# Performance work log

Hardware: AMD Instinct MI355X
Metric: run time of the kernel (lower is better)

The kernel has to match this reference:

```python
import jax, jax.numpy as jnp
import numpy as np

N = 50000      # nodes
E = 800000     # edges (avg degree 16)
D_IN, D_H, D_OUT = 128, 256, 128


def setup_inputs() -> dict:
    key = jax.random.key(0)
    ks = jax.random.split(key, 8)
    x = jax.random.normal(ks[0], (N, D_IN), dtype=jnp.float32)
    edge_index = jax.random.randint(ks[1], (2, E), 0, N, dtype=jnp.int64)
    s1 = 1.0 / np.sqrt(D_IN).astype(np.float32)
    s2 = 1.0 / np.sqrt(D_H).astype(np.float32)
    return {
        "x": x,
        "edge_index": edge_index,
        "W1l": jax.random.normal(ks[2], (D_H, D_IN), jnp.float32) * s1,
        "b1l": jnp.zeros((D_H,), jnp.float32),
        "W1r": jax.random.normal(ks[3], (D_H, D_IN), jnp.float32) * s1,
        "W2l": jax.random.normal(ks[4], (D_OUT, D_H), jnp.float32) * s2,
        "b2l": jnp.zeros((D_OUT,), jnp.float32),
        "W2r": jax.random.normal(ks[5], (D_OUT, D_H), jnp.float32) * s2,
    }


def sage_conv(x, src, dst, Wl, bl, Wr):
    # mean-aggregate source features into destination nodes
    agg = jax.ops.segment_sum(x[src], dst, num_segments=N)           # [N, d_in]
    deg = jax.ops.segment_sum(jnp.ones((src.shape[0],), x.dtype), dst, num_segments=N)
    mean = agg / jnp.maximum(deg, 1.0)[:, None]
    # lin_l(mean_agg) + lin_r(x_root); lin_r has no bias (PyG SAGEConv default)
    return mean @ Wl.T + bl + x @ Wr.T


def reference(x, edge_index, W1l, b1l, W1r, W2l, b2l, W2r):
    src, dst = edge_index[0], edge_index[1]
    h = sage_conv(x, src, dst, W1l, b1l, W1r)
    h = jax.nn.relu(h)  # dropout inactive in eval mode
    return sage_conv(h, src, dst, W2l, b2l, W2r)
```

## Files before the change

kernel.cpp:

```cpp
#include <hip/hip_runtime.h>


typedef __attribute__((ext_vector_type(8))) short bf16x8;
typedef __attribute__((ext_vector_type(4))) float floatx4;

__device__ inline unsigned short f2b(float f) {
  unsigned int x = __float_as_uint(f);
  unsigned int r = (x + 0x7fffu + ((x >> 16) & 1u)) >> 16;
  return (unsigned short)r;
}
__device__ inline float blo(unsigned int u) { return __uint_as_float(u << 16); }
__device__ inline float bhi(unsigned int u) { return __uint_as_float(u & 0xffff0000u); }

#define ACC8(A, u)                                            \
  {                                                           \
    A[0] += blo((u).x); A[1] += bhi((u).x);                   \
    A[2] += blo((u).y); A[3] += bhi((u).y);                   \
    A[4] += blo((u).z); A[5] += bhi((u).z);                   \
    A[6] += blo((u).w); A[7] += bhi((u).w);                   \
  }

__global__ void prep_kernel(const float* __restrict__ x,
                            const float* __restrict__ W1l, const float* __restrict__ W1r,
                            const float* __restrict__ W2l, const float* __restrict__ W2r,
                            unsigned short* __restrict__ Wc1, unsigned short* __restrict__ Wc2,
                            unsigned short* __restrict__ A1,
                            int* __restrict__ cnt, int* __restrict__ off, int N, int E) {
  int i = blockIdx.x * blockDim.x + threadIdx.x;
  if (i < 65536) {
    int j = i >> 8, k = i & 255;
    float v1 = (k < 128) ? W1l[j * 128 + k] : W1r[j * 128 + (k - 128)];
    Wc1[i] = f2b(v1);
    float v2 = (j < 128) ? W2l[j * 256 + k] : W2r[(j - 128) * 256 + k];
    Wc2[i] = f2b(v2);
  }
  if (i < N) cnt[i] = 0;
  if (i == 0) off[N] = E;
  if (i < N * 32) {
    int n = i >> 5, c = (i & 31) * 4;
    float4 v = *(const float4*)(x + (size_t)n * 128 + c);
    uint2 p;
    p.x = (unsigned int)f2b(v.x) | ((unsigned int)f2b(v.y) << 16);
    p.y = (unsigned int)f2b(v.z) | ((unsigned int)f2b(v.w) << 16);
    *(uint2*)(A1 + (size_t)n * 256 + 128 + c) = p;
  }
}

__global__ void hist_kernel(const int* __restrict__ dst, int* __restrict__ cnt,
                            int* __restrict__ rank, int E) {
  int i = blockIdx.x * blockDim.x + threadIdx.x;
  int e = i * 4;
  if (e + 3 < E) {
    int4 d = *(const int4*)(dst + e);
    int4 r;
    r.x = atomicAdd(&cnt[d.x], 1);
    r.y = atomicAdd(&cnt[d.y], 1);
    r.z = atomicAdd(&cnt[d.z], 1);
    r.w = atomicAdd(&cnt[d.w], 1);
    *(int4*)(rank + e) = r;
  } else {
    for (; e < E; e++) rank[e] = atomicAdd(&cnt[dst[e]], 1);
  }
}

__global__ __launch_bounds__(1024) void scan_blocks_kernel(const int* __restrict__ cnt,
                                                           int* __restrict__ off,
                                                           int* __restrict__ bsum, int N) {
  __shared__ int wsum[16];
  __shared__ int wincl[16];
  const int tid = threadIdx.x;
  const int lane = tid & 63;
  const int wv = tid >> 6;
  const int i = blockIdx.x * 1024 + tid;
  const int v = (i < N) ? cnt[i] : 0;
  int s = v;
#pragma unroll
  for (int o = 1; o < 64; o <<= 1) {
    int t = __shfl_up(s, o, 64);
    if (lane >= o) s += t;
  }
  if (lane == 63) wsum[wv] = s;
  __syncthreads();
  if (tid < 16) {
    int ws = wsum[tid];
#pragma unroll
    for (int o = 1; o < 16; o <<= 1) {
      int t = __shfl_up(ws, o, 16);
      if ((tid & 15) >= o) ws += t;
    }
    wincl[tid] = ws;
  }
  __syncthreads();
  const int wo = wv ? wincl[wv - 1] : 0;
  if (i < N) off[i] = wo + s - v;
  if (tid == 1023) bsum[blockIdx.x] = wo + s;
}

__global__ __launch_bounds__(1024) void scan_add_kernel(int* __restrict__ off,
                                                        const int* __restrict__ bsum, int N, int SB) {
  __shared__ int bofs[64];
  const int tid = threadIdx.x;
  if (tid < 64) {
    int v = (tid < SB) ? bsum[tid] : 0;
    int s = v;
#pragma unroll
    for (int o = 1; o < 64; o <<= 1) {
      int t = __shfl_up(s, o, 64);
      if (tid >= o) s += t;
    }
    bofs[tid] = s - v;
  }
  __syncthreads();
  int i = blockIdx.x * 1024 + tid;
  if (i < N) off[i] = off[i] + bofs[blockIdx.x];
}

__global__ void fill_kernel(const int* __restrict__ src, const int* __restrict__ dst,
                            const int* __restrict__ rank, const int* __restrict__ off,
                            int* __restrict__ csr, int E) {
  int i = blockIdx.x * blockDim.x + threadIdx.x;
  int e = i * 4;
  if (e + 3 < E) {
    int4 d = *(const int4*)(dst + e);
    int4 r = *(const int4*)(rank + e);
    int4 s = *(const int4*)(src + e);
    csr[off[d.x] + r.x] = s.x;
    csr[off[d.y] + r.y] = s.y;
    csr[off[d.z] + r.z] = s.z;
    csr[off[d.w] + r.w] = s.w;
  } else {
    for (; e < E; e++) csr[off[dst[e]] + rank[e]] = src[e];
  }
}

__global__ void gather1_kernel(const unsigned short* __restrict__ feat,
                               const int* __restrict__ csr, const int* __restrict__ off,
                               unsigned short* __restrict__ ob, int N) {
  int wid = (blockIdx.x * blockDim.x + threadIdx.x) >> 6;
  if (wid >= N) return;
  const int lane = threadIdx.x & 63;
  const int slot = lane >> 3;
  const int j = lane & 7;
  const int c0 = j * 8;
  const int s0 = off[wid], s1 = off[wid + 1];
  float a[16] = {};
  int e = s0 + slot;
  for (; e + 8 < s1; e += 16) {
    int i0 = csr[e], i1 = csr[e + 8];
    uint4 u0 = *(const uint4*)(feat + (size_t)i0 * 256 + c0);
    uint4 v0 = *(const uint4*)(feat + (size_t)i0 * 256 + 64 + c0);
    uint4 u1 = *(const uint4*)(feat + (size_t)i1 * 256 + c0);
    uint4 v1 = *(const uint4*)(feat + (size_t)i1 * 256 + 64 + c0);
    ACC8(a, u0); ACC8((a + 8), v0);
    ACC8(a, u1); ACC8((a + 8), v1);
  }
  for (; e < s1; e += 8) {
    int i0 = csr[e];
    uint4 u0 = *(const uint4*)(feat + (size_t)i0 * 256 + c0);
    uint4 v0 = *(const uint4*)(feat + (size_t)i0 * 256 + 64 + c0);
    ACC8(a, u0); ACC8((a + 8), v0);
  }
#pragma unroll
  for (int k = 0; k < 16; k++) {
    a[k] += __shfl_xor(a[k], 8, 64);
    a[k] += __shfl_xor(a[k], 16, 64);
    a[k] += __shfl_xor(a[k], 32, 64);
  }
  if (slot == 0) {
    const float inv = 1.0f / fmaxf((float)(s1 - s0), 1.0f);
    uint4 p;
    p.x = (unsigned int)f2b(a[0] * inv) | ((unsigned int)f2b(a[1] * inv) << 16);
    p.y = (unsigned int)f2b(a[2] * inv) | ((unsigned int)f2b(a[3] * inv) << 16);
    p.z = (unsigned int)f2b(a[4] * inv) | ((unsigned int)f2b(a[5] * inv) << 16);
    p.w = (unsigned int)f2b(a[6] * inv) | ((unsigned int)f2b(a[7] * inv) << 16);
    *(uint4*)(ob + (size_t)wid * 256 + c0) = p;
    p.x = (unsigned int)f2b(a[8] * inv) | ((unsigned int)f2b(a[9] * inv) << 16);
    p.y = (unsigned int)f2b(a[10] * inv) | ((unsigned int)f2b(a[11] * inv) << 16);
    p.z = (unsigned int)f2b(a[12] * inv) | ((unsigned int)f2b(a[13] * inv) << 16);
    p.w = (unsigned int)f2b(a[14] * inv) | ((unsigned int)f2b(a[15] * inv) << 16);
    *(uint4*)(ob + (size_t)wid * 256 + 64 + c0) = p;
  }
}

__global__ void gather2_kernel(const unsigned short* __restrict__ t,
                               const int* __restrict__ csr, const int* __restrict__ off,
                               float* __restrict__ out, int N) {
  int wid = (blockIdx.x * blockDim.x + threadIdx.x) >> 6;
  if (wid >= N) return;
  const int lane = threadIdx.x & 63;
  const int slot = lane >> 3;
  const int j = lane & 7;
  const int c0 = j * 8;
  const int s0 = off[wid], s1 = off[wid + 1];
  float a[16] = {};
  int e = s0 + slot;
  for (; e + 8 < s1; e += 16) {
    int i0 = csr[e], i1 = csr[e + 8];
    uint4 u0 = *(const uint4*)(t + (size_t)i0 * 128 + c0);
    uint4 v0 = *(const uint4*)(t + (size_t)i0 * 128 + 64 + c0);
    uint4 u1 = *(const uint4*)(t + (size_t)i1 * 128 + c0);
    uint4 v1 = *(const uint4*)(t + (size_t)i1 * 128 + 64 + c0);
    ACC8(a, u0); ACC8((a + 8), v0);
    ACC8(a, u1); ACC8((a + 8), v1);
  }
  for (; e < s1; e += 8) {
    int i0 = csr[e];
    uint4 u0 = *(const uint4*)(t + (size_t)i0 * 128 + c0);
    uint4 v0 = *(const uint4*)(t + (size_t)i0 * 128 + 64 + c0);
    ACC8(a, u0); ACC8((a + 8), v0);
  }
#pragma unroll
  for (int k = 0; k < 16; k++) {
    a[k] += __shfl_xor(a[k], 8, 64);
    a[k] += __shfl_xor(a[k], 16, 64);
    a[k] += __shfl_xor(a[k], 32, 64);
  }
  if (slot == 0) {
    const float inv = 1.0f / fmaxf((float)(s1 - s0), 1.0f);
    float4* o0 = (float4*)(out + (size_t)wid * 128 + c0);
    float4* o1 = (float4*)(out + (size_t)wid * 128 + 64 + c0);
    float4 r0 = o0[0], r1 = o0[1], r2 = o1[0], r3 = o1[1];
    r0.x += a[0] * inv;  r0.y += a[1] * inv;  r0.z += a[2] * inv;  r0.w += a[3] * inv;
    r1.x += a[4] * inv;  r1.y += a[5] * inv;  r1.z += a[6] * inv;  r1.w += a[7] * inv;
    r2.x += a[8] * inv;  r2.y += a[9] * inv;  r2.z += a[10] * inv; r2.w += a[11] * inv;
    r3.x += a[12] * inv; r3.y += a[13] * inv; r3.z += a[14] * inv; r3.w += a[15] * inv;
    o0[0] = r0; o0[1] = r1; o1[0] = r2; o1[1] = r3;
  }
}

__global__ __launch_bounds__(512, 4)
void gemm1(const unsigned short* __restrict__ A, const unsigned short* __restrict__ Wc1,
           const float* __restrict__ b1, unsigned short* __restrict__ H, int M) {
  constexpr int LDA = 264;
  __shared__ __align__(16) unsigned short As[64 * LDA];
  const int t = threadIdx.x;
  const int lane = t & 63;
  const int wave = t >> 6;
  const int wn = wave * 32;
  const int l15 = lane & 15;
  const int quad = lane >> 4;
  const int m_blk = blockIdx.x * 64;

  bf16x8 wr[2][8];
#pragma unroll
  for (int nt = 0; nt < 2; nt++) {
    const unsigned short* wp = Wc1 + (size_t)(wn + nt * 16 + l15) * 256 + quad * 8;
#pragma unroll
    for (int c = 0; c < 8; c++) wr[nt][c] = *(const bf16x8*)(wp + c * 32);
  }
  const float bv0 = b1[wn + l15];
  const float bv1 = b1[wn + 16 + l15];

#pragma unroll
  for (int i = 0; i < 4; i++) {
    int idx = t + 512 * i;
    int row = idx >> 5, cc = (idx & 31) * 8;
    int ar = m_blk + row;
    if (ar >= M) ar = M - 1;
    *(uint4*)(As + row * LDA + cc) = *(const uint4*)(A + (size_t)ar * 256 + cc);
  }
  __syncthreads();

  floatx4 acc[4][2] = {};
#pragma unroll
  for (int c = 0; c < 8; c++) {
    bf16x8 af[4];
#pragma unroll
    for (int mt = 0; mt < 4; mt++)
      af[mt] = *(const bf16x8*)(As + (mt * 16 + l15) * LDA + c * 32 + quad * 8);
#pragma unroll
    for (int mt = 0; mt < 4; mt++) {
      acc[mt][0] = __builtin_amdgcn_mfma_f32_16x16x32_bf16(af[mt], wr[0][c], acc[mt][0], 0, 0, 0);
      acc[mt][1] = __builtin_amdgcn_mfma_f32_16x16x32_bf16(af[mt], wr[1][c], acc[mt][1], 0, 0, 0);
    }
  }

#pragma unroll
  for (int mt = 0; mt < 4; mt++) {
#pragma unroll
    for (int nt = 0; nt < 2; nt++) {
      const int j = wn + nt * 16 + l15;
      const float bv = nt ? bv1 : bv0;
#pragma unroll
      for (int r = 0; r < 4; r++) {
        const int node = m_blk + mt * 16 + quad * 4 + r;
        if (node < M) H[(size_t)node * 256 + j] = f2b(fmaxf(acc[mt][nt][r] + bv, 0.f));
      }
    }
  }
}

__global__ __launch_bounds__(512, 4)
void gemm2(const unsigned short* __restrict__ H, const unsigned short* __restrict__ Wc2,
           const float* __restrict__ b2, unsigned short* __restrict__ tb,
           float* __restrict__ out, int M) {
  constexpr int LDA = 264;
  __shared__ __align__(16) unsigned short As[64 * LDA];
  const int t = threadIdx.x;
  const int lane = t & 63;
  const int wave = t >> 6;
  const int wn = wave * 32;
  const int l15 = lane & 15;
  const int quad = lane >> 4;
  const int m_blk = blockIdx.x * 64;

  bf16x8 wr[2][8];
#pragma unroll
  for (int nt = 0; nt < 2; nt++) {
    const unsigned short* wp = Wc2 + (size_t)(wn + nt * 16 + l15) * 256 + quad * 8;
#pragma unroll
    for (int c = 0; c < 8; c++) wr[nt][c] = *(const bf16x8*)(wp + c * 32);
  }
  const float bv0 = (wn >= 128) ? b2[wn - 128 + l15] : 0.f;
  const float bv1 = (wn >= 128) ? b2[wn - 112 + l15] : 0.f;

#pragma unroll
  for (int i = 0; i < 4; i++) {
    int idx = t + 512 * i;
    int row = idx >> 5, cc = (idx & 31) * 8;
    int ar = m_blk + row;
    if (ar >= M) ar = M - 1;
    *(uint4*)(As + row * LDA + cc) = *(const uint4*)(H + (size_t)ar * 256 + cc);
  }
  __syncthreads();

  floatx4 acc[4][2] = {};
#pragma unroll
  for (int c = 0; c < 8; c++) {
    bf16x8 af[4];
#pragma unroll
    for (int mt = 0; mt < 4; mt++)
      af[mt] = *(const bf16x8*)(As + (mt * 16 + l15) * LDA + c * 32 + quad * 8);
#pragma unroll
    for (int mt = 0; mt < 4; mt++) {
      acc[mt][0] = __builtin_amdgcn_mfma_f32_16x16x32_bf16(af[mt], wr[0][c], acc[mt][0], 0, 0, 0);
      acc[mt][1] = __builtin_amdgcn_mfma_f32_16x16x32_bf16(af[mt], wr[1][c], acc[mt][1], 0, 0, 0);
    }
  }

#pragma unroll
  for (int mt = 0; mt < 4; mt++) {
#pragma unroll
    for (int nt = 0; nt < 2; nt++) {
      const int j = wn + nt * 16 + l15;
      const float bv = nt ? bv1 : bv0;
#pragma unroll
      for (int r = 0; r < 4; r++) {
        const int node = m_blk + mt * 16 + quad * 4 + r;
        if (node >= M) continue;
        const float v = acc[mt][nt][r];
        if (j < 128) {
          tb[(size_t)node * 128 + j] = f2b(v);
        } else {
          out[(size_t)node * 128 + (j - 128)] = v + bv;
        }
      }
    }
  }
}

extern "C" void kernel_launch(void* const* d_in, const int* in_sizes, int n_in,
                              void* d_out, int out_size, void* d_ws, size_t ws_size,
                              hipStream_t stream) {
  const float* x   = (const float*)d_in[0];
  const int*  eidx = (const int*)d_in[1];
  const float* W1l = (const float*)d_in[2];
  const float* b1l = (const float*)d_in[3];
  const float* W1r = (const float*)d_in[4];
  const float* W2l = (const float*)d_in[5];
  const float* b2l = (const float*)d_in[6];
  const float* W2r = (const float*)d_in[7];
  float* out = (float*)d_out;

  const int N = in_sizes[0] / 128;
  const int E = in_sizes[1] / 2;
  const int* src = eidx;
  const int* dst = eidx + E;

  int* cnt  = (int*)d_ws;
  int* off  = cnt + N;
  int* bsum = off + N + 1;
  int* rank = bsum + 64;
  int* csr  = rank + E;
  size_t ioff = ((size_t)(N + N + 1 + 64 + 2 * E) * 4 + 15) & ~(size_t)15;
  unsigned short* A1  = (unsigned short*)((char*)d_ws + ioff);
  unsigned short* h   = A1 + (size_t)N * 256;
  unsigned short* tb  = h + (size_t)N * 256;
  unsigned short* Wc1 = tb + (size_t)N * 128;
  unsigned short* Wc2 = Wc1 + 65536;

  const int SB = (N + 1023) / 1024;

  prep_kernel<<<(N * 32 + 255) / 256, 256, 0, stream>>>(x, W1l, W1r, W2l, W2r,
                                                        Wc1, Wc2, A1, cnt, off, N, E);
  hist_kernel<<<(E / 4 + 255) / 256, 256, 0, stream>>>(dst, cnt, rank, E);
  scan_blocks_kernel<<<SB, 1024, 0, stream>>>(cnt, off, bsum, N);
  scan_add_kernel<<<SB, 1024, 0, stream>>>(off, bsum, N, SB);
  fill_kernel<<<(E / 4 + 255) / 256, 256, 0, stream>>>(src, dst, rank, off, csr, E);

  const int gblocks = (N + 3) / 4;
  gather1_kernel<<<gblocks, 256, 0, stream>>>(A1 + 128, csr, off, A1, N);

  const int mblocks = (N + 63) / 64;
  gemm1<<<mblocks, 512, 0, stream>>>(A1, Wc1, b1l, h, N);
  gemm2<<<mblocks, 512, 0, stream>>>(h, Wc2, b2l, tb, out, N);

  gather2_kernel<<<gblocks, 256, 0, stream>>>(tb, csr, off, out, N);
}
```

Baseline: 275.8 us.

## Fuse both GEMMs via shared-memory hidden tile and restructure gathers per-lane

The two GEMM kernels become one: the ReLU'd hidden tile is written to a second shared-memory buffer and fed straight into the second GEMM, so the bf16 hidden matrix no longer makes a round trip through global memory. The gather kernels also change layout. Each wave now loads a chunk of up to 64 neighbor indices at once, broadcasts them with shuffles, and has every lane read a 4-byte column pair per neighbor. This removes the cross-slot shuffle reductions but processes only one neighbor row per load step, unrolled by 4. The fused kernel doubles shared memory per block, which may lower occupancy.

```diff
diff --git a/kernel.cpp b/kernel.cpp
--- a/kernel.cpp
+++ b/kernel.cpp
@@ -11,14 +11,6 @@
 }
 __device__ inline float blo(unsigned int u) { return __uint_as_float(u << 16); }
 __device__ inline float bhi(unsigned int u) { return __uint_as_float(u & 0xffff0000u); }
-
-#define ACC8(A, u)                                            \
-  {                                                           \
-    A[0] += blo((u).x); A[1] += bhi((u).x);                   \
-    A[2] += blo((u).y); A[3] += bhi((u).y);                   \
-    A[4] += blo((u).z); A[5] += bhi((u).z);                   \
-    A[6] += blo((u).w); A[7] += bhi((u).w);                   \
-  }
 
 __global__ void prep_kernel(const float* __restrict__ x,
                             const float* __restrict__ W1l, const float* __restrict__ W1r,
@@ -139,47 +131,35 @@
   int wid = (blockIdx.x * blockDim.x + threadIdx.x) >> 6;
   if (wid >= N) return;
   const int lane = threadIdx.x & 63;
-  const int slot = lane >> 3;
-  const int j = lane & 7;
-  const int c0 = j * 8;
   const int s0 = off[wid], s1 = off[wid + 1];
-  float a[16] = {};
-  int e = s0 + slot;
-  for (; e + 8 < s1; e += 16) {
-    int i0 = csr[e], i1 = csr[e + 8];
-    uint4 u0 = *(const uint4*)(feat + (size_t)i0 * 256 + c0);
-    uint4 v0 = *(const uint4*)(feat + (size_t)i0 * 256 + 64 + c0);
-    uint4 u1 = *(const uint4*)(feat + (size_t)i1 * 256 + c0);
-    uint4 v1 = *(const uint4*)(feat + (size_t)i1 * 256 + 64 + c0);
-    ACC8(a, u0); ACC8((a + 8), v0);
-    ACC8(a, u1); ACC8((a + 8), v1);
-  }
-  for (; e < s1; e += 8) {
-    int i0 = csr[e];
-    uint4 u0 = *(const uint4*)(feat + (size_t)i0 * 256 + c0);
-    uint4 v0 = *(const uint4*)(feat + (size_t)i0 * 256 + 64 + c0);
-    ACC8(a, u0); ACC8((a + 8), v0);
-  }
-#pragma unroll
-  for (int k = 0; k < 16; k++) {
-    a[k] += __shfl_xor(a[k], 8, 64);
-    a[k] += __shfl_xor(a[k], 16, 64);
-    a[k] += __shfl_xor(a[k], 32, 64);
-  }
-  if (slot == 0) {
-    const float inv = 1.0f / fmaxf((float)(s1 - s0), 1.0f);
-    uint4 p;
-    p.x = (unsigned int)f2b(a[0] * inv) | ((unsigned int)f2b(a[1] * inv) << 16);
-    p.y = (unsigned int)f2b(a[2] * inv) | ((unsigned int)f2b(a[3] * inv) << 16);
-    p.z = (unsigned int)f2b(a[4] * inv) | ((unsigned int)f2b(a[5] * inv) << 16);
-    p.w = (unsigned int)f2b(a[6] * inv) | ((unsigned int)f2b(a[7] * inv) << 16);
-    *(uint4*)(ob + (size_t)wid * 256 + c0) = p;
-    p.x = (unsigned int)f2b(a[8] * inv) | ((unsigned int)f2b(a[9] * inv) << 16);
-    p.y = (unsigned int)f2b(a[10] * inv) | ((unsigned int)f2b(a[11] * inv) << 16);
-    p.z = (unsigned int)f2b(a[12] * inv) | ((unsigned int)f2b(a[13] * inv) << 16);
-    p.w = (unsigned int)f2b(a[14] * inv) | ((unsigned int)f2b(a[15] * inv) << 16);
-    *(uint4*)(ob + (size_t)wid * 256 + 64 + c0) = p;
-  }
+  float a0 = 0.f, a1 = 0.f;
+  for (int base = s0; base < s1; base += 64) {
+    const int cnt = min(64, s1 - base);
+    int my = (lane < cnt) ? csr[base + lane] : 0;
+    int k = 0;
+    for (; k + 4 <= cnt; k += 4) {
+      int i0 = __shfl(my, k);
+      int i1 = __shfl(my, k + 1);
+      int i2 = __shfl(my, k + 2);
+      int i3 = __shfl(my, k + 3);
+      unsigned u0 = ((const unsigned*)(feat + (size_t)i0 * 256))[lane];
+      unsigned u1 = ((const unsigned*)(feat + (size_t)i1 * 256))[lane];
+      unsigned u2 = ((const unsigned*)(feat + (size_t)i2 * 256))[lane];
+      unsigned u3 = ((const unsigned*)(feat + (size_t)i3 * 256))[lane];
+      a0 += blo(u0); a1 += bhi(u0);
+      a0 += blo(u1); a1 += bhi(u1);
+      a0 += blo(u2); a1 += bhi(u2);
+      a0 += blo(u3); a1 += bhi(u3);
+    }
+    for (; k < cnt; k++) {
+      int i0 = __shfl(my, k);
+      unsigned u0 = ((const unsigned*)(feat + (size_t)i0 * 256))[lane];
+      a0 += blo(u0); a1 += bhi(u0);
+    }
+  }
+  const float inv = 1.0f / fmaxf((float)(s1 - s0), 1.0f);
+  unsigned p = (unsigned)f2b(a0 * inv) | ((unsigned)f2b(a1 * inv) << 16);
+  ((unsigned*)(ob + (size_t)wid * 256))[lane] = p;
 }
 
 __global__ void gather2_kernel(const unsigned short* __restrict__ t,
@@ -188,51 +168,48 @@
   int wid = (blockIdx.x * blockDim.x + threadIdx.x) >> 6;
   if (wid >= N) return;
   const int lane = threadIdx.x & 63;
-  const int slot = lane >> 3;
-  const int j = lane & 7;
-  const int c0 = j * 8;
   const int s0 = off[wid], s1 = off[wid + 1];
-  float a[16] = {};
-  int e = s0 + slot;
-  for (; e + 8 < s1; e += 16) {
-    int i0 = csr[e], i1 = csr[e + 8];
-    uint4 u0 = *(const uint4*)(t + (size_t)i0 * 128 + c0);
-    uint4 v0 = *(const uint4*)(t + (size_t)i0 * 128 + 64 + c0);
-    uint4 u1 = *(const uint4*)(t + (size_t)i1 * 128 + c0);
-    uint4 v1 = *(const uint4*)(t + (size_t)i1 * 128 + 64 + c0);
-    ACC8(a, u0); ACC8((a + 8), v0);
-    ACC8(a, u1); ACC8((a + 8), v1);
-  }
-  for (; e < s1; e += 8) {
-    int i0 = csr[e];
-    uint4 u0 = *(const uint4*)(t + (size_t)i0 * 128 + c0);
-    uint4 v0 = *(const uint4*)(t + (size_t)i0 * 128 + 64 + c0);
-    ACC8(a, u0); ACC8((a + 8), v0);
-  }
-#pragma unroll
-  for (int k = 0; k < 16; k++) {
-    a[k] += __shfl_xor(a[k], 8, 64);
-    a[k] += __shfl_xor(a[k], 16, 64);
-    a[k] += __shfl_xor(a[k], 32, 64);
-  }
-  if (slot == 0) {
-    const float inv = 1.0f / fmaxf((float)(s1 - s0), 1.0f);
-    float4* o0 = (float4*)(out + (size_t)wid * 128 + c0);
-    float4* o1 = (float4*)(out + (size_t)wid * 128 + 64 + c0);
-    float4 r0 = o0[0], r1 = o0[1], r2 = o1[0], r3 = o1[1];
-    r0.x += a[0] * inv;  r0.y += a[1] * inv;  r0.z += a[2] * inv;  r0.w += a[3] * inv;
-    r1.x += a[4] * inv;  r1.y += a[5] * inv;  r1.z += a[6] * inv;  r1.w += a[7] * inv;
-    r2.x += a[8] * inv;  r2.y += a[9] * inv;  r2.z += a[10] * inv; r2.w += a[11] * inv;
-    r3.x += a[12] * inv; r3.y += a[13] * inv; r3.z += a[14] * inv; r3.w += a[15] * inv;
-    o0[0] = r0; o0[1] = r1; o1[0] = r2; o1[1] = r3;
-  }
+  float a0 = 0.f, a1 = 0.f;
+  for (int base = s0; base < s1; base += 64) {
+    const int cnt = min(64, s1 - base);
+    int my = (lane < cnt) ? csr[base + lane] : 0;
+    int k = 0;
+    for (; k + 4 <= cnt; k += 4) {
+      int i0 = __shfl(my, k);
+      int i1 = __shfl(my, k + 1);
+      int i2 = __shfl(my, k + 2);
+      int i3 = __shfl(my, k + 3);
+      unsigned u0 = ((const unsigned*)(t + (size_t)i0 * 128))[lane];
+      unsigned u1 = ((const unsigned*)(t + (size_t)i1 * 128))[lane];
+      unsigned u2 = ((const unsigned*)(t + (size_t)i2 * 128))[lane];
+      unsigned u3 = ((const unsigned*)(t + (size_t)i3 * 128))[lane];
+      a0 += blo(u0); a1 += bhi(u0);
+      a0 += blo(u1); a1 += bhi(u1);
+      a0 += blo(u2); a1 += bhi(u2);
+      a0 += blo(u3); a1 += bhi(u3);
+    }
+    for (; k < cnt; k++) {
+      int i0 = __shfl(my, k);
+      unsigned u0 = ((const unsigned*)(t + (size_t)i0 * 128))[lane];
+      a0 += blo(u0); a1 += bhi(u0);
+    }
+  }
+  const float inv = 1.0f / fmaxf((float)(s1 - s0), 1.0f);
+  float2* op = (float2*)(out + (size_t)wid * 128) + lane;
+  float2 r = *op;
+  r.x += a0 * inv;
+  r.y += a1 * inv;
+  *op = r;
 }
 
 __global__ __launch_bounds__(512, 4)
-void gemm1(const unsigned short* __restrict__ A, const unsigned short* __restrict__ Wc1,
-           const float* __restrict__ b1, unsigned short* __restrict__ H, int M) {
+void gemm_fused(const unsigned short* __restrict__ A, const unsigned short* __restrict__ Wc1,
+                const unsigned short* __restrict__ Wc2,
+                const float* __restrict__ b1, const float* __restrict__ b2,
+                unsigned short* __restrict__ tb, float* __restrict__ out, int M) {
   constexpr int LDA = 264;
   __shared__ __align__(16) unsigned short As[64 * LDA];
+  __shared__ __align__(16) unsigned short Hs[64 * LDA];
   const int t = threadIdx.x;
   const int lane = t & 63;
   const int wave = t >> 6;
@@ -279,58 +256,37 @@
   for (int mt = 0; mt < 4; mt++) {
 #pragma unroll
     for (int nt = 0; nt < 2; nt++) {
-      const int j = wn + nt * 16 + l15;
+      const int jl = wn + nt * 16 + l15;
       const float bv = nt ? bv1 : bv0;
 #pragma unroll
       for (int r = 0; r < 4; r++) {
-        const int node = m_blk + mt * 16 + quad * 4 + r;
-        if (node < M) H[(size_t)node * 256 + j] = f2b(fmaxf(acc[mt][nt][r] + bv, 0.f));
+        const int row = mt * 16 + quad * 4 + r;
+        Hs[row * LDA + jl] = f2b(fmaxf(acc[mt][nt][r] + bv, 0.f));
       }
     }
   }
-}
-
-__global__ __launch_bounds__(512, 4)
-void gemm2(const unsigned short* __restrict__ H, const unsigned short* __restrict__ Wc2,
-           const float* __restrict__ b2, unsigned short* __restrict__ tb,
-           float* __restrict__ out, int M) {
-  constexpr int LDA = 264;
-  __shared__ __align__(16) unsigned short As[64 * LDA];
-  const int t = threadIdx.x;
-  const int lane = t & 63;
-  const int wave = t >> 6;
-  const int wn = wave * 32;
-  const int l15 = lane & 15;
-  const int quad = lane >> 4;
-  const int m_blk = blockIdx.x * 64;
-
-  bf16x8 wr[2][8];
+
 #pragma unroll
   for (int nt = 0; nt < 2; nt++) {
     const unsigned short* wp = Wc2 + (size_t)(wn + nt * 16 + l15) * 256 + quad * 8;
 #pragma unroll
     for (int c = 0; c < 8; c++) wr[nt][c] = *(const bf16x8*)(wp + c * 32);
   }
-  const float bv0 = (wn >= 128) ? b2[wn - 128 + l15] : 0.f;
-  const float bv1 = (wn >= 128) ? b2[wn - 112 + l15] : 0.f;
-
-#pragma unroll
-  for (int i = 0; i < 4; i++) {
-    int idx = t + 512 * i;
-    int row = idx >> 5, cc = (idx & 31) * 8;
-    int ar = m_blk + row;
-    if (ar >= M) ar = M - 1;
-    *(uint4*)(As + row * LDA + cc) = *(const uint4*)(H + (size_t)ar * 256 + cc);
-  }
-  __syncthreads();
-
-  floatx4 acc[4][2] = {};
+  const float cv0 = (wn >= 128) ? b2[wn - 128 + l15] : 0.f;
+  const float cv1 = (wn >= 128) ? b2[wn - 112 + l15] : 0.f;
+  __syncthreads();
+
+#pragma unroll
+  for (int mt = 0; mt < 4; mt++) {
+    acc[mt][0] = (floatx4){0.f, 0.f, 0.f, 0.f};
+    acc[mt][1] = (floatx4){0.f, 0.f, 0.f, 0.f};
+  }
 #pragma unroll
   for (int c = 0; c < 8; c++) {
     bf16x8 af[4];
 #pragma unroll
     for (int mt = 0; mt < 4; mt++)
-      af[mt] = *(const bf16x8*)(As + (mt * 16 + l15) * LDA + c * 32 + quad * 8);
+      af[mt] = *(const bf16x8*)(Hs + (mt * 16 + l15) * LDA + c * 32 + quad * 8);
 #pragma unroll
     for (int mt = 0; mt < 4; mt++) {
       acc[mt][0] = __builtin_amdgcn_mfma_f32_16x16x32_bf16(af[mt], wr[0][c], acc[mt][0], 0, 0, 0);
@@ -343,7 +299,7 @@
 #pragma unroll
     for (int nt = 0; nt < 2; nt++) {
       const int j = wn + nt * 16 + l15;
-      const float bv = nt ? bv1 : bv0;
+      const float bv = nt ? cv1 : cv0;
 #pragma unroll
       for (int r = 0; r < 4; r++) {
         const int node = m_blk + mt * 16 + quad * 4 + r;
@@ -384,8 +340,7 @@
   int* csr  = rank + E;
   size_t ioff = ((size_t)(N + N + 1 + 64 + 2 * E) * 4 + 15) & ~(size_t)15;
   unsigned short* A1  = (unsigned short*)((char*)d_ws + ioff);
-  unsigned short* h   = A1 + (size_t)N * 256;
-  unsigned short* tb  = h + (size_t)N * 256;
+  unsigned short* tb  = A1 + (size_t)N * 256;
   unsigned short* Wc1 = tb + (size_t)N * 128;
   unsigned short* Wc2 = Wc1 + 65536;
 
@@ -401,9 +356,7 @@
   const int gblocks = (N + 3) / 4;
   gather1_kernel<<<gblocks, 256, 0, stream>>>(A1 + 128, csr, off, A1, N);
 
-  const int mblocks = (N + 63) / 64;
-  gemm1<<<mblocks, 512, 0, stream>>>(A1, Wc1, b1l, h, N);
-  gemm2<<<mblocks, 512, 0, stream>>>(h, Wc2, b2l, tb, out, N);
+  gemm_fused<<<(N + 63) / 64, 512, 0, stream>>>(A1, Wc1, Wc2, b1l, b2l, tb, out, N);
 
   gather2_kernel<<<gblocks, 256, 0, stream>>>(tb, csr, off, out, N);
 }
```

Result: faster. 267.8 us (-2.9%).
